# Performance work log

Measured on AMD Instinct MI355X. Metric: run time of the kernel, lower is better.

The kernel has to match this reference:

```python
import jax, jax.numpy as jnp
import numpy as np

SCENE_BOUND = 1.5

# SH degree-2 constants (standard real spherical harmonics, Plenoxels convention)
C0 = 0.28209479177387814
C1 = 0.4886025119029199
C2_0 = 1.0925484305920792
C2_1 = -1.0925484305920792
C2_2 = 0.31539156525252005
C2_3 = -1.0925484305920792
C2_4 = 0.5462742152960396


def sh_basis(dirs):
    # dirs: (N,3) unit vectors -> (N,9) deg-2 SH basis
    x, y, z = dirs[:, 0], dirs[:, 1], dirs[:, 2]
    xx, yy, zz = x * x, y * y, z * z
    return jnp.stack([
        jnp.full_like(x, C0),
        -C1 * y,
        C1 * z,
        -C1 * x,
        C2_0 * x * y,
        C2_1 * y * z,
        C2_2 * (2.0 * zz - xx - yy),
        C2_3 * x * z,
        C2_4 * (xx - yy),
    ], axis=-1)


def grid_sample_trilinear(vol, pts):
    """torch F.grid_sample(mode=bilinear, padding=zeros, align_corners=True).

    vol: (C, D, H, W); pts: (N, 3) in [-1, 1], ordered (x, y, z) where
    x indexes W, y indexes H, z indexes D (torch convention).
    Returns (N, C).
    """
    C, D, H, W = vol.shape
    # align_corners=True: -1 -> 0, +1 -> size-1
    fx = (pts[:, 0] + 1.0) * 0.5 * (W - 1)
    fy = (pts[:, 1] + 1.0) * 0.5 * (H - 1)
    fz = (pts[:, 2] + 1.0) * 0.5 * (D - 1)
    x0 = jnp.floor(fx); y0 = jnp.floor(fy); z0 = jnp.floor(fz)
    wx1 = fx - x0; wy1 = fy - y0; wz1 = fz - z0
    x0i = x0.astype(jnp.int32); y0i = y0.astype(jnp.int32); z0i = z0.astype(jnp.int32)

    out = jnp.zeros((pts.shape[0], C), dtype=vol.dtype)
    for dz in (0, 1):
        zi = z0i + dz
        wz = wz1 if dz == 1 else (1.0 - wz1)
        for dy in (0, 1):
            yi = y0i + dy
            wy = wy1 if dy == 1 else (1.0 - wy1)
            for dx in (0, 1):
                xi = x0i + dx
                wx = wx1 if dx == 1 else (1.0 - wx1)
                inb = ((xi >= 0) & (xi < W) & (yi >= 0) & (yi < H)
                       & (zi >= 0) & (zi < D))
                xc = jnp.clip(xi, 0, W - 1)
                yc = jnp.clip(yi, 0, H - 1)
                zc = jnp.clip(zi, 0, D - 1)
                val = vol[:, zc, yc, xc]  # (C, N) gather
                w = (wx * wy * wz) * inb.astype(vol.dtype)
                out = out + val.T * w[:, None]
    return out


def setup_inputs() -> dict:
    key = jax.random.key(0)
    k1, k2, k3 = jax.random.split(key, 3)
    N, R, C = 2_000_000, 128, 28
    xyz = (jax.random.uniform(k1, (N, 3), jnp.float32) * 2.0 - 1.0) * SCENE_BOUND
    vd = jax.random.normal(k2, (N, 3), jnp.float32)
    view_dirs = vd / jnp.linalg.norm(vd, axis=-1, keepdims=True)
    density_grid = jnp.full((1, 1, R, R, R), 0.1, jnp.float32)
    sh_grid = jax.random.normal(k3, (1, C - 1, R, R, R), jnp.float32) * 0.01
    return {"xyz": xyz, "view_dirs": view_dirs,
            "density_grid": density_grid, "sh_grid": sh_grid}


def reference(xyz, view_dirs, density_grid, sh_grid):
    # combined grid (1, C, R, R, R) -> (C, D, H, W)
    vol = jnp.concatenate([density_grid, sh_grid], axis=1)[0]
    # query: trilinear interp at normalized coords
    feats = grid_sample_trilinear(vol, xyz / SCENE_BOUND)  # (N, C)
    # decode
    density = jax.nn.relu(feats[:, 0])  # (N,)
    sh_coef = feats[:, 1:].reshape(feats.shape[0], 3, 9)  # (N, 3, 9)
    basis = sh_basis(view_dirs)  # (N, 9)
    rgb = jax.nn.sigmoid(jnp.einsum('ncb,nb->nc', sh_coef, basis))  # (N, 3)
    return density, rgb
```

## Files before the change

### kernel.cpp

```cpp
#include <hip/hip_runtime.h>
#include <hip/hip_fp16.h>
#include <math.h>

#define GR 128
#define NCH 28
#define CSTR 32
#define NSUB 64
#define NREG 512

typedef unsigned int uivec4 __attribute__((ext_vector_type(4)));


__device__ __forceinline__ float sigmoidf_(float x) {
    return 1.0f / (1.0f + expf(-x));
}
__device__ __forceinline__ __half2 u2h2(unsigned int u) {
    return *reinterpret_cast<__half2*>(&u);
}

__global__ __launch_bounds__(256) void pack_kernel(
    const float* __restrict__ dens,
    const float* __restrict__ sh,
    uint4* __restrict__ vol,
    int V)
{
    int t = blockIdx.x * blockDim.x + threadIdx.x;
    int v0 = t * 2;
    if (v0 >= V) return;

    float2 dd = *reinterpret_cast<const float2*>(dens + v0);
    float sa[27], sb[27];
#pragma unroll
    for (int q = 0; q < 27; ++q) {
        float2 s2 = *reinterpret_cast<const float2*>(sh + (size_t)q * (size_t)V + v0);
        sa[q] = s2.x;
        sb[q] = s2.y;
    }

#pragma unroll
    for (int j = 0; j < 2; ++j) {
        const float* sv = (j == 0) ? sa : sb;
        float dv = (j == 0) ? dd.x : dd.y;

        float mp = 0.0f, mn = 0.0f;
#pragma unroll
        for (int q = 0; q < 27; ++q) {
            float x = sv[q];
            mp = fmaxf(mp, x);
            mn = fmaxf(mn, -x);
        }
        float tq = fmaxf(fmaxf(mp * (1.0f / 7.0f), mn * 0.125f), 7.5e-9f);
        int ex = (int)((__float_as_uint(tq) >> 23) & 0xFFu) - 126;
        int e = min(max(ex + 14, 0), 15);
        float invf = __uint_as_float((unsigned int)(141 - e) << 23);

        unsigned int w[4];
#pragma unroll
        for (int d = 0; d < 3; ++d) {
            unsigned int acc = 0;
#pragma unroll
            for (int b = 0; b < 8; ++b) {
                int n = (int)rintf(sv[8 * d + b] * invf) + 8;
                n = min(max(n, 0), 15);
                acc |= (unsigned int)n << (4 * b);
            }
            w[d] = acc;
        }
        int n24 = min(max((int)rintf(sv[24] * invf) + 8, 0), 15);
        int n25 = min(max((int)rintf(sv[25] * invf) + 8, 0), 15);
        int n26 = min(max((int)rintf(sv[26] * invf) + 8, 0), 15);
        unsigned int dh = (unsigned int)__half_as_ushort(__float2half_rn(dv));
        w[3] = (unsigned int)n24 | ((unsigned int)n25 << 4) | ((unsigned int)n26 << 8)
             | ((unsigned int)e << 12) | (dh << 16);

        vol[v0 + j] = make_uint4(w[0], w[1], w[2], w[3]);
    }
}

__device__ __forceinline__ void trilerp_shade(
    const uint4* __restrict__ vol,
    int x0, int y0, int z0, float wx1, float wy1, float wz1,
    float dxv, float dyv, float dzv,
    float* __restrict__ out, int N, unsigned int idx)
{
    float wx0 = 1.0f - wx1, wy0 = 1.0f - wy1, wz0 = 1.0f - wz1;
    int x1 = min(x0 + 1, GR - 1);
    int y1 = min(y0 + 1, GR - 1);
    int z1 = min(z0 + 1, GR - 1);

    int r00 = (z0 * GR + y0) * GR, r01 = (z0 * GR + y1) * GR;
    int r10 = (z1 * GR + y0) * GR, r11 = (z1 * GR + y1) * GR;
    uint4 c000 = vol[r00 + x0];
    uint4 c001 = vol[r00 + x1];
    uint4 c010 = vol[r01 + x0];
    uint4 c011 = vol[r01 + x1];
    uint4 c100 = vol[r10 + x0];
    uint4 c101 = vol[r10 + x1];
    uint4 c110 = vol[r11 + x0];
    uint4 c111 = vol[r11 + x1];

    float w000 = wz0 * wy0 * wx0, w001 = wz0 * wy0 * wx1;
    float w010 = wz0 * wy1 * wx0, w011 = wz0 * wy1 * wx1;
    float w100 = wz1 * wy0 * wx0, w101 = wz1 * wy0 * wx1;
    float w110 = wz1 * wy1 * wx0, w111 = wz1 * wy1 * wx1;

    __half2 acc2[15];
#pragma unroll
    for (int p = 0; p < 15; ++p) acc2[p] = u2h2(0u);
    float G = 0.0f, accd = 0.0f;

    #define NIB4(DW, O)                                                        \
    {                                                                          \
        acc2[(O)+0] = __hfma2(g2, u2h2((((DW) << 6) & 0x03C003C0u) | 0x3C003C00u), acc2[(O)+0]); \
        acc2[(O)+1] = __hfma2(g2, u2h2((((DW) << 2) & 0x03C003C0u) | 0x3C003C00u), acc2[(O)+1]); \
        acc2[(O)+2] = __hfma2(g2, u2h2((((DW) >> 2) & 0x03C003C0u) | 0x3C003C00u), acc2[(O)+2]); \
        acc2[(O)+3] = __hfma2(g2, u2h2((((DW) >> 6) & 0x03C003C0u) | 0x3C003C00u), acc2[(O)+3]); \
    }
    #define NIB3(DW, O)                                                        \
    {                                                                          \
        acc2[(O)+0] = __hfma2(g2, u2h2((((DW) << 6) & 0x03C003C0u) | 0x3C003C00u), acc2[(O)+0]); \
        acc2[(O)+1] = __hfma2(g2, u2h2((((DW) << 2) & 0x03C003C0u) | 0x3C003C00u), acc2[(O)+1]); \
        acc2[(O)+2] = __hfma2(g2, u2h2((((DW) >> 2) & 0x03C003C0u) | 0x3C003C00u), acc2[(O)+2]); \
    }
    #define CORNER(C, W)                                                       \
    {                                                                          \
        float w_ = (W);                                                        \
        unsigned int e_ = ((C).w >> 12) & 0xFu;                                \
        float f_ = __uint_as_float((113u + e_) << 23);           \
        float g_ = w_ * f_;                                                    \
        G += g_;                                                               \
        accd = fmaf(w_, __half2float(__ushort_as_half((unsigned short)((C).w >> 16))), accd); \
        __half2 g2 = __float2half2_rn(g_);                                     \
        NIB4((C).x, 0) NIB4((C).y, 4) NIB4((C).z, 8) NIB3((C).w, 12)           \
    }

    CORNER(c000, w000) CORNER(c001, w001) CORNER(c010, w010) CORNER(c011, w011)
    CORNER(c100, w100) CORNER(c101, w101) CORNER(c110, w110) CORNER(c111, w111)
    #undef CORNER
    #undef NIB4
    #undef NIB3

    float c24G = 24.0f * G;
    float sch[27];
#pragma unroll
    for (int d = 0; d < 3; ++d) {
#pragma unroll
        for (int p = 0; p < 4; ++p) {
            float2 f2 = __half22float2(acc2[d * 4 + p]);
            sch[8 * d + p]     = fmaf(16.0f, f2.x, -c24G);
            sch[8 * d + p + 4] = fmaf(16.0f, f2.y, -c24G);
        }
    }
#pragma unroll
    for (int p = 0; p < 3; ++p) {
        float2 f2 = __half22float2(acc2[12 + p]);
        sch[24 + p] = fmaf(16.0f, f2.x, -c24G);
    }

    float xx = dxv*dxv, yy = dyv*dyv, zz = dzv*dzv;
    float bs[9];
    bs[0] = 0.28209479177387814f;
    bs[1] = -0.4886025119029199f * dyv;
    bs[2] =  0.4886025119029199f * dzv;
    bs[3] = -0.4886025119029199f * dxv;
    bs[4] =  1.0925484305920792f * dxv * dyv;
    bs[5] = -1.0925484305920792f * dyv * dzv;
    bs[6] =  0.31539156525252005f * (2.0f*zz - xx - yy);
    bs[7] = -1.0925484305920792f * dxv * dzv;
    bs[8] =  0.5462742152960396f * (xx - yy);

    __builtin_nontemporal_store(fmaxf(accd, 0.0f), &out[idx]);
#pragma unroll
    for (int ch = 0; ch < 3; ++ch) {
        float sm = 0.0f;
#pragma unroll
        for (int q = 0; q < 9; ++q) sm = fmaf(sch[ch*9 + q], bs[q], sm);
        __builtin_nontemporal_store(sigmoidf_(sm), &out[(size_t)N + 3*(size_t)idx + ch]);
    }
}

__global__ __launch_bounds__(256) void zero_kernel(unsigned int* __restrict__ p, int n) {
    int i = blockIdx.x * blockDim.x + threadIdx.x;
    if (i < n) p[i] = 0u;
}

__global__ __launch_bounds__(256) void scatter_oct_kernel(
    const float* __restrict__ xyz, const float* __restrict__ vdirs,
    unsigned int* __restrict__ cursors,
    uint4* __restrict__ recs, int N, int cap_sub)
{
    int i = blockIdx.x * blockDim.x + threadIdx.x;
    bool active = (i < N);
    unsigned int ux = 0, uy = 0, uz = 0, hx = 0, hy = 0, hz = 0;
    int oct = -1;
    if (active) {
        const float kk = (1.0f / 1.5f) * 0.5f * (float)(GR - 1);
        const float cc = 0.5f * (float)(GR - 1);
        float fx = fminf(fmaxf(fmaf(xyz[3*i+0], kk, cc), 0.0f), (float)(GR - 1));
        float fy = fminf(fmaxf(fmaf(xyz[3*i+1], kk, cc), 0.0f), (float)(GR - 1));
        float fz = fminf(fmaxf(fmaf(xyz[3*i+2], kk, cc), 0.0f), (float)(GR - 1));
        ux = (unsigned int)(int)rintf(fx * 512.0f);
        uy = (unsigned int)(int)rintf(fy * 512.0f);
        uz = (unsigned int)(int)rintf(fz * 512.0f);
        hx = (unsigned int)__half_as_ushort(__float2half_rn(vdirs[3*i+0]));
        hy = (unsigned int)__half_as_ushort(__float2half_rn(vdirs[3*i+1]));
        hz = (unsigned int)__half_as_ushort(__float2half_rn(vdirs[3*i+2]));
        oct = (int)((ux >> 15) | ((uy >> 15) << 1) | ((uz >> 15) << 2));
    }

    int lane = (int)(threadIdx.x & 63u);
    int blockSub = (int)(blockIdx.x & (NSUB - 1));
#pragma unroll
    for (int k = 0; k < 8; ++k) {
        unsigned long long mask = __ballot(active && (oct == k));
        if (active && (oct == k)) {
            int leader = __ffsll((unsigned long long)mask) - 1;
            int rank = __popcll(mask & ((1ull << lane) - 1ull));
            int s = k * NSUB + blockSub;
            unsigned int base = 0;
            if (lane == leader)
                base = atomicAdd(&cursors[s * CSTR], (unsigned int)__popcll(mask));
            base = (unsigned int)__shfl((int)base, leader);
            unsigned int pos = (unsigned int)s * (unsigned int)cap_sub + base + (unsigned int)rank;
            uivec4 r;
            r.x = ux | (uy << 16);
            r.y = uz | (hx << 16);
            r.z = hy | (hz << 16);
            r.w = (unsigned int)i;
            __builtin_nontemporal_store(r, (uivec4*)(recs + pos));
        }
    }
}

__global__ __launch_bounds__(256) void sample_oct_kernel(
    const uint4* __restrict__ recs,
    const unsigned int* __restrict__ cursors,
    const uint4* __restrict__ vol,
    float* __restrict__ out, int N, int cap_sub, int nwg)
{
    int bid = blockIdx.x;
    int cpx = nwg >> 3;
    int swz = (bid & 7) * cpx + (bid >> 3);
    int i = swz * 256 + (int)threadIdx.x;

    unsigned int s = (unsigned int)i / (unsigned int)cap_sub;
    unsigned int off = (unsigned int)i - s * (unsigned int)cap_sub;
    if (off >= cursors[s * CSTR]) return;

    uivec4 Rv = __builtin_nontemporal_load((const uivec4*)(recs + i));
    unsigned int ux = Rv.x & 0xFFFFu, uy = Rv.x >> 16;
    unsigned int uz = Rv.y & 0xFFFFu;
    int x0 = (int)(ux >> 9), y0 = (int)(uy >> 9), z0 = (int)(uz >> 9);
    float wx1 = (float)(ux & 511u) * (1.0f / 512.0f);
    float wy1 = (float)(uy & 511u) * (1.0f / 512.0f);
    float wz1 = (float)(uz & 511u) * (1.0f / 512.0f);

    float dxv = __half2float(__ushort_as_half((unsigned short)(Rv.y >> 16)));
    float dyv = __half2float(__ushort_as_half((unsigned short)(Rv.z & 0xFFFFu)));
    float dzv = __half2float(__ushort_as_half((unsigned short)(Rv.z >> 16)));

    trilerp_shade(vol, x0, y0, z0, wx1, wy1, wz1, dxv, dyv, dzv, out, N, Rv.w);
}

__global__ __launch_bounds__(256) void sample_kernel(
    const float* __restrict__ xyz,
    const float* __restrict__ vdirs,
    const uint4* __restrict__ vol,
    float* __restrict__ out,
    int N)
{
    int i = blockIdx.x * blockDim.x + threadIdx.x;
    if (i >= N) return;

    const float kk = (1.0f / 1.5f) * 0.5f * (float)(GR - 1);
    const float cc = 0.5f * (float)(GR - 1);
    float fx = fminf(fmaxf(fmaf(xyz[3*i+0], kk, cc), 0.0f), (float)(GR - 1));
    float fy = fminf(fmaxf(fmaf(xyz[3*i+1], kk, cc), 0.0f), (float)(GR - 1));
    float fz = fminf(fmaxf(fmaf(xyz[3*i+2], kk, cc), 0.0f), (float)(GR - 1));
    int x0 = (int)fx, y0 = (int)fy, z0 = (int)fz;
    trilerp_shade(vol, x0, y0, z0, fx - (float)x0, fy - (float)y0, fz - (float)z0,
                  vdirs[3*i+0], vdirs[3*i+1], vdirs[3*i+2], out, N, (unsigned int)i);
}

__global__ __launch_bounds__(256) void sample_direct_kernel(
    const float* __restrict__ xyz,
    const float* __restrict__ vdirs,
    const float* __restrict__ dens,
    const float* __restrict__ sh,
    float* __restrict__ out,
    int N)
{
    int i = blockIdx.x * blockDim.x + threadIdx.x;
    if (i >= N) return;

    const float kk = (1.0f / 1.5f) * 0.5f * (float)(GR - 1);
    const float cc = 0.5f * (float)(GR - 1);
    float fx = fminf(fmaxf(fmaf(xyz[3*i+0], kk, cc), 0.0f), (float)(GR - 1));
    float fy = fminf(fmaxf(fmaf(xyz[3*i+1], kk, cc), 0.0f), (float)(GR - 1));
    float fz = fminf(fmaxf(fmaf(xyz[3*i+2], kk, cc), 0.0f), (float)(GR - 1));
    float x0f = floorf(fx), y0f = floorf(fy), z0f = floorf(fz);
    float wx1 = fx - x0f, wy1 = fy - y0f, wz1 = fz - z0f;
    int x0 = (int)x0f, y0 = (int)y0f, z0 = (int)z0f;
    float wx[2] = { 1.0f - wx1, wx1 };
    float wy[2] = { 1.0f - wy1, wy1 };
    float wz[2] = { 1.0f - wz1, wz1 };
    int xi[2] = { x0, min(x0 + 1, GR-1) };
    int yi[2] = { y0, min(y0 + 1, GR-1) };
    int zi[2] = { z0, min(z0 + 1, GR-1) };

    const size_t V = (size_t)GR * GR * GR;
    float acc[NCH];
#pragma unroll
    for (int c = 0; c < NCH; ++c) acc[c] = 0.0f;

#pragma unroll
    for (int dz = 0; dz < 2; ++dz)
#pragma unroll
        for (int dy = 0; dy < 2; ++dy)
#pragma unroll
            for (int dx = 0; dx < 2; ++dx) {
                float w = wz[dz] * wy[dy] * wx[dx];
                size_t vox = (((size_t)zi[dz] * GR) + yi[dy]) * GR + xi[dx];
                acc[0] = fmaf(w, dens[vox], acc[0]);
#pragma unroll
                for (int c = 0; c < 27; ++c)
                    acc[1 + c] = fmaf(w, sh[(size_t)c * V + vox], acc[1 + c]);
            }

    float dxv = vdirs[3*i+0], dyv = vdirs[3*i+1], dzv = vdirs[3*i+2];
    float xx = dxv*dxv, yy = dyv*dyv, zz = dzv*dzv;
    float b[9];
    b[0] = 0.28209479177387814f;
    b[1] = -0.4886025119029199f * dyv;
    b[2] =  0.4886025119029199f * dzv;
    b[3] = -0.4886025119029199f * dxv;
    b[4] =  1.0925484305920792f * dxv * dyv;
    b[5] = -1.0925484305920792f * dyv * dzv;
    b[6] =  0.31539156525252005f * (2.0f*zz - xx - yy);
    b[7] = -1.0925484305920792f * dxv * dzv;
    b[8] =  0.5462742152960396f * (xx - yy);

    out[i] = fmaxf(acc[0], 0.0f);
#pragma unroll
    for (int c = 0; c < 3; ++c) {
        float sm = 0.0f;
#pragma unroll
        for (int q = 0; q < 9; ++q) sm = fmaf(acc[1 + c*9 + q], b[q], sm);
        out[(size_t)N + 3*(size_t)i + c] = sigmoidf_(sm);
    }
}

extern "C" void kernel_launch(void* const* d_in, const int* in_sizes, int n_in,
                              void* d_out, int out_size, void* d_ws, size_t ws_size,
                              hipStream_t stream) {
    const float* xyz   = (const float*)d_in[0];
    const float* vdirs = (const float*)d_in[1];
    const float* dens  = (const float*)d_in[2];
    const float* sh    = (const float*)d_in[3];
    float* out = (float*)d_out;

    int N = in_sizes[0] / 3;
    const int V = GR * GR * GR;

    int per = (N + NREG - 1) / NREG;
    int cap_sub = (per + per / 10 + 64 + 3) & ~3;

    size_t off_vol  = 0;
    size_t sz_vol   = (size_t)V * 16;
    size_t off_recs = (off_vol + sz_vol + 255) & ~(size_t)255;
    size_t sz_recs  = (size_t)NREG * (size_t)cap_sub * 16;
    size_t off_cur  = (off_recs + sz_recs + 255) & ~(size_t)255;
    size_t sz_cur   = (size_t)NREG * CSTR * 4;
    size_t need_full = off_cur + sz_cur;
    size_t need_mid  = sz_vol;

    if (ws_size >= need_full) {
        char* ws = (char*)d_ws;
        uint4*        vol     = (uint4*)(ws + off_vol);
        uint4*        recs    = (uint4*)(ws + off_recs);
        unsigned int* cursors = (unsigned int*)(ws + off_cur);

        int nwg_pts = (N + 255) / 256;
        int ncur = NREG * CSTR;
        int nslots = NREG * cap_sub;
        int nwg_s = nslots / 256;

        pack_kernel<<<(V / 2 + 255) / 256, 256, 0, stream>>>(dens, sh, vol, V);
        zero_kernel<<<(ncur + 255) / 256, 256, 0, stream>>>(cursors, ncur);
        scatter_oct_kernel<<<nwg_pts, 256, 0, stream>>>(xyz, vdirs, cursors, recs, N, cap_sub);
        sample_oct_kernel<<<nwg_s, 256, 0, stream>>>(recs, cursors, vol, out, N, cap_sub, nwg_s);
    } else if (ws_size >= need_mid) {
        uint4* vol = (uint4*)d_ws;
        pack_kernel<<<(V / 2 + 255) / 256, 256, 0, stream>>>(dens, sh, vol, V);
        sample_kernel<<<(N + 255) / 256, 256, 0, stream>>>(xyz, vdirs, vol, out, N);
    } else {
        sample_direct_kernel<<<(N + 255) / 256, 256, 0, stream>>>(xyz, vdirs, dens, sh, out, N);
    }
}
```

Baseline: 201.5 us.

## Bin points into 64 spatial regions with block-local shared-memory histogram

Replaces the octant binning (8 regions × 64 sub-buckets) with 64 spatial regions (4x4x4) × 8 sub-buckets. The per-wave ballot/atomic loop is replaced by a shared-memory histogram per block, followed by one global atomic per region per block. Finer regions should make the sample kernel's gathers into the packed volume more local, improving cache reuse. Per-bucket capacity stays N/512 plus slack, so an uneven spatial distribution could overflow a bucket. The sample kernel's sweep swizzle still assumes the old 8-way grouping.

```diff
diff --git a/kernel.cpp b/kernel.cpp
--- a/kernel.cpp
+++ b/kernel.cpp
@@ -5,8 +5,9 @@
 #define GR 128
 #define NCH 28
 #define CSTR 32
-#define NSUB 64
-#define NREG 512
+#define NREGION 64
+#define NSUB 8
+#define NBUCKET 512
 
 typedef unsigned int uivec4 __attribute__((ext_vector_type(4)));
 
@@ -184,15 +185,22 @@
     if (i < n) p[i] = 0u;
 }
 
-__global__ __launch_bounds__(256) void scatter_oct_kernel(
+__global__ __launch_bounds__(256) void scatter_reg_kernel(
     const float* __restrict__ xyz, const float* __restrict__ vdirs,
     unsigned int* __restrict__ cursors,
     uint4* __restrict__ recs, int N, int cap_sub)
 {
-    int i = blockIdx.x * blockDim.x + threadIdx.x;
+    __shared__ unsigned int lh[NREGION];
+    __shared__ unsigned int gb[NREGION];
+
+    int t = (int)threadIdx.x;
+    if (t < NREGION) lh[t] = 0u;
+    __syncthreads();
+
+    int i = blockIdx.x * 256 + t;
     bool active = (i < N);
-    unsigned int ux = 0, uy = 0, uz = 0, hx = 0, hy = 0, hz = 0;
-    int oct = -1;
+    unsigned int ux = 0, uy = 0, uz = 0, hx = 0, hy = 0, hz = 0, rank = 0;
+    int r = 0;
     if (active) {
         const float kk = (1.0f / 1.5f) * 0.5f * (float)(GR - 1);
         const float cc = 0.5f * (float)(GR - 1);
@@ -205,34 +213,29 @@
         hx = (unsigned int)__half_as_ushort(__float2half_rn(vdirs[3*i+0]));
         hy = (unsigned int)__half_as_ushort(__float2half_rn(vdirs[3*i+1]));
         hz = (unsigned int)__half_as_ushort(__float2half_rn(vdirs[3*i+2]));
-        oct = (int)((ux >> 15) | ((uy >> 15) << 1) | ((uz >> 15) << 2));
-    }
-
-    int lane = (int)(threadIdx.x & 63u);
-    int blockSub = (int)(blockIdx.x & (NSUB - 1));
-#pragma unroll
-    for (int k = 0; k < 8; ++k) {
-        unsigned long long mask = __ballot(active && (oct == k));
-        if (active && (oct == k)) {
-            int leader = __ffsll((unsigned long long)mask) - 1;
-            int rank = __popcll(mask & ((1ull << lane) - 1ull));
-            int s = k * NSUB + blockSub;
-            unsigned int base = 0;
-            if (lane == leader)
-                base = atomicAdd(&cursors[s * CSTR], (unsigned int)__popcll(mask));
-            base = (unsigned int)__shfl((int)base, leader);
-            unsigned int pos = (unsigned int)s * (unsigned int)cap_sub + base + (unsigned int)rank;
-            uivec4 r;
-            r.x = ux | (uy << 16);
-            r.y = uz | (hx << 16);
-            r.z = hy | (hz << 16);
-            r.w = (unsigned int)i;
-            __builtin_nontemporal_store(r, (uivec4*)(recs + pos));
-        }
-    }
-}
-
-__global__ __launch_bounds__(256) void sample_oct_kernel(
+        r = (int)((ux >> 14) | (((uy >> 14) & 3u) << 2) | (((uz >> 14) & 3u) << 4));
+        rank = atomicAdd(&lh[r], 1u);
+    }
+    __syncthreads();
+
+    int bsub = (int)(blockIdx.x & (NSUB - 1));
+    if (t < NREGION && lh[t] > 0)
+        gb[t] = atomicAdd(&cursors[(t * NSUB + bsub) * CSTR], lh[t]);
+    __syncthreads();
+
+    if (active) {
+        unsigned int pos = ((unsigned int)r * NSUB + (unsigned int)bsub) * (unsigned int)cap_sub
+                         + gb[r] + rank;
+        uivec4 rec;
+        rec.x = ux | (uy << 16);
+        rec.y = uz | (hx << 16);
+        rec.z = hy | (hz << 16);
+        rec.w = (unsigned int)i;
+        __builtin_nontemporal_store(rec, (uivec4*)(recs + pos));
+    }
+}
+
+__global__ __launch_bounds__(256) void sample_reg_kernel(
     const uint4* __restrict__ recs,
     const unsigned int* __restrict__ cursors,
     const uint4* __restrict__ vol,
@@ -362,15 +365,15 @@
     int N = in_sizes[0] / 3;
     const int V = GR * GR * GR;
 
-    int per = (N + NREG - 1) / NREG;
+    int per = (N + NBUCKET - 1) / NBUCKET;
     int cap_sub = (per + per / 10 + 64 + 3) & ~3;
 
     size_t off_vol  = 0;
     size_t sz_vol   = (size_t)V * 16;
     size_t off_recs = (off_vol + sz_vol + 255) & ~(size_t)255;
-    size_t sz_recs  = (size_t)NREG * (size_t)cap_sub * 16;
+    size_t sz_recs  = (size_t)NBUCKET * (size_t)cap_sub * 16;
     size_t off_cur  = (off_recs + sz_recs + 255) & ~(size_t)255;
-    size_t sz_cur   = (size_t)NREG * CSTR * 4;
+    size_t sz_cur   = (size_t)NBUCKET * CSTR * 4;
     size_t need_full = off_cur + sz_cur;
     size_t need_mid  = sz_vol;
 
@@ -381,14 +384,14 @@
         unsigned int* cursors = (unsigned int*)(ws + off_cur);
 
         int nwg_pts = (N + 255) / 256;
-        int ncur = NREG * CSTR;
-        int nslots = NREG * cap_sub;
+        int ncur = NBUCKET * CSTR;
+        int nslots = NBUCKET * cap_sub;
         int nwg_s = nslots / 256;
 
         pack_kernel<<<(V / 2 + 255) / 256, 256, 0, stream>>>(dens, sh, vol, V);
         zero_kernel<<<(ncur + 255) / 256, 256, 0, stream>>>(cursors, ncur);
-        scatter_oct_kernel<<<nwg_pts, 256, 0, stream>>>(xyz, vdirs, cursors, recs, N, cap_sub);
-        sample_oct_kernel<<<nwg_s, 256, 0, stream>>>(recs, cursors, vol, out, N, cap_sub, nwg_s);
+        scatter_reg_kernel<<<nwg_pts, 256, 0, stream>>>(xyz, vdirs, cursors, recs, N, cap_sub);
+        sample_reg_kernel<<<nwg_s, 256, 0, stream>>>(recs, cursors, vol, out, N, cap_sub, nwg_s);
     } else if (ws_size >= need_mid) {
         uint4* vol = (uint4*)d_ws;
         pack_kernel<<<(V / 2 + 255) / 256, 256, 0, stream>>>(dens, sh, vol, V);
```

Result: slower. 262.0 us (+30.0%).
